# Optimization experiments

Hardware: AMD Instinct MI355X
Metric: run time of the kernel (lower is better)

## Reference

```python
import jax, jax.numpy as jnp
import numpy as np

N = 20000      # nodes (single node type)
E = 320000     # edges per relation (avg degree 16)
R = 3          # relations / edge types
L = 3          # layers
H = 4          # heads
D = 64         # dim per head (hid_size // n_heads)
IN = 256       # in_size == hid_size
OUT = 128      # out_size
NEG_SLOPE = 0.2


def setup_inputs() -> dict:
    key = jax.random.key(0)
    ks = jax.random.split(key, 8)
    x = jax.random.normal(ks[0], (N, IN), jnp.float32)
    edge_src = jax.random.randint(ks[1], (R, E), 0, N, dtype=jnp.int32)
    edge_dst = jax.random.randint(ks[2], (R, E), 0, N, dtype=jnp.int32)
    W = jax.random.normal(ks[3], (L, R, IN, H * D), jnp.float32) * (1.0 / np.sqrt(IN))
    attn_l = jax.random.normal(ks[4], (L, R, H, D), jnp.float32) * 0.1
    attn_r = jax.random.normal(ks[5], (L, R, H, D), jnp.float32) * 0.1
    bias = jnp.zeros((L, R, H * D), jnp.float32)
    fc_w = jax.random.normal(ks[6], (IN, OUT), jnp.float32) * (1.0 / np.sqrt(IN))
    fc_b = jnp.zeros((OUT,), jnp.float32)
    return dict(x=x, edge_src=edge_src, edge_dst=edge_dst, W=W,
                attn_l=attn_l, attn_r=attn_r, bias=bias, fc_w=fc_w, fc_b=fc_b)


def _gat_conv(h, src, dst, W_r, al, ar, b_r):
    # h: [N, IN] -> feat: [N, H, D]
    feat = (h @ W_r).reshape(N, H, D)
    el = jnp.sum(feat * al, axis=-1)                      # [N, H]
    er = jnp.sum(feat * ar, axis=-1)                      # [N, H]
    e = jax.nn.leaky_relu(el[src] + er[dst], NEG_SLOPE)   # [E, H]
    # segment softmax over incoming edges of each dst node, per head
    m = jax.ops.segment_max(e, dst, num_segments=N)       # [N, H]
    a = jnp.exp(e - m[dst])
    s = jax.ops.segment_sum(a, dst, num_segments=N)       # [N, H]
    alpha = a / s[dst]                                    # [E, H]
    # weighted scatter-add of source features: [N, H, D]
    out = jax.ops.segment_sum(alpha[:, :, None] * feat[src], dst, num_segments=N)
    return out + b_r.reshape(1, H, D)


def reference(x, edge_src, edge_dst, W, attn_l, attn_r, bias, fc_w, fc_b):
    h = x
    for l in range(L):
        acc = jnp.zeros((N, H, D), h.dtype)
        for r in range(R):  # sum-aggregate across relations (HeteroGraphConv aggregate='sum')
            acc = acc + _gat_conv(h, edge_src[r], edge_dst[r],
                                  W[l, r], attn_l[l, r], attn_r[l, r], bias[l, r])
        h = acc.reshape(N, H * D)
        if l != L - 1:
            h = jax.nn.relu(h)  # dropout = identity in eval
    return h @ fc_w + fc_b  # [N, OUT]
```

## Files before the change

kernel.cpp:

```cpp
#include <hip/hip_runtime.h>
#include <math.h>

#define NN 20000
#define EE 320000
#define RR 3
#define LL 3
#define HH 4
#define DD 64
#define CDIM 256
#define OUTD 128
#define NEG 0.2f

typedef float f32x4 __attribute__((ext_vector_type(4)));
typedef short sh8 __attribute__((ext_vector_type(8)));

__device__ __forceinline__ ushort f2bf(float f) {
    union { float f; uint u; } v; v.f = f;
    uint r = (v.u + 0x7FFF + ((v.u >> 16) & 1)) >> 16;
    return (ushort)r;
}
__device__ __forceinline__ float bf2f(ushort u) {
    union { uint u; float f; } v; v.u = ((uint)u) << 16;
    return v.f;
}
__device__ __forceinline__ float bflo(uint p) { return bf2f((ushort)(p & 0xffff)); }
__device__ __forceinline__ float bfhi(uint p) { return bf2f((ushort)(p >> 16)); }


__global__ void zero_ints(int* p, int n) {
    int i = blockIdx.x * blockDim.x + threadIdx.x;
    if (i < n) p[i] = 0;
}

__global__ void count_deg(const int* __restrict__ edge_dst, int* __restrict__ deg) {
    int i = blockIdx.x * blockDim.x + threadIdx.x;
    if (i >= RR * EE) return;
    int r = i / EE;
    atomicAdd(&deg[r * NN + edge_dst[i]], 1);
}

__global__ void scan_kernel(const int* __restrict__ deg, int* __restrict__ row_ptr) {
    int r = blockIdx.x;
    const int* d = deg + r * NN;
    int* rp = row_ptr + r * (NN + 1);
    __shared__ int buf[1024];
    __shared__ int carry_s;
    if (threadIdx.x == 0) { carry_s = 0; rp[0] = 0; }
    __syncthreads();
    for (int base = 0; base < NN; base += 1024) {
        int i = base + threadIdx.x;
        int v = (i < NN) ? d[i] : 0;
        buf[threadIdx.x] = v;
        __syncthreads();
        for (int off = 1; off < 1024; off <<= 1) {
            int t = (threadIdx.x >= off) ? buf[threadIdx.x - off] : 0;
            __syncthreads();
            buf[threadIdx.x] += t;
            __syncthreads();
        }
        int incl = carry_s + buf[threadIdx.x];
        if (i < NN) rp[i + 1] = incl;
        __syncthreads();
        if (threadIdx.x == 1023) carry_s = carry_s + buf[1023];
        __syncthreads();
    }
}

__global__ void fill_csr(const int* __restrict__ edge_src, const int* __restrict__ edge_dst,
                         const int* __restrict__ row_ptr, int* __restrict__ fill,
                         int* __restrict__ csr_src) {
    int i = blockIdx.x * blockDim.x + threadIdx.x;
    if (i >= RR * EE) return;
    int r = i / EE;
    int dst = edge_dst[i];
    int pos = atomicAdd(&fill[r * NN + dst], 1);
    csr_src[r * EE + row_ptr[r * (NN + 1) + dst] + pos] = edge_src[i];
}


__global__ void cvt_bf16x4(const float* __restrict__ in, ushort* __restrict__ out, int n4) {
    int i = blockIdx.x * blockDim.x + threadIdx.x;
    if (i >= n4) return;
    float4 v = *(const float4*)(in + (size_t)i * 4);
    ushort4 o;
    o.x = f2bf(v.x); o.y = f2bf(v.y); o.z = f2bf(v.z); o.w = f2bf(v.w);
    *(ushort4*)(out + (size_t)i * 4) = o;
}

__global__ void prep_Wt(const float* __restrict__ W, ushort* __restrict__ Wt, int K, int N) {
    __shared__ float tile[32][33];
    int kb = blockIdx.x * 32, nb = blockIdx.y * 32;
    size_t base = (size_t)blockIdx.z * K * N;
    for (int yy = threadIdx.y; yy < 32; yy += 8)
        tile[yy][threadIdx.x] = W[base + (size_t)(kb + yy) * N + nb + threadIdx.x];
    __syncthreads();
    for (int yy = threadIdx.y; yy < 32; yy += 8)
        Wt[base + (size_t)(nb + yy) * K + kb + threadIdx.x] = f2bf(tile[threadIdx.x][yy]);
}


#define TM 128
#define TN 128
#define TK 32
#define LP 40

__global__ __launch_bounds__(256) void gemm_bf16(
    const ushort* __restrict__ A, const ushort* __restrict__ Bt0, void* __restrict__ C0,
    int M, int K, int Ncol, long strideB, long strideC,
    const float* __restrict__ bias, int out_fp32) {
    __shared__ alignas(16) ushort As[TM * LP];
    __shared__ alignas(16) ushort Bs[TN * LP];
    const ushort* Bt = Bt0 + (size_t)blockIdx.z * strideB;
    int m0 = blockIdx.x * TM, n0 = blockIdx.y * TN;
    int t = threadIdx.x;
    int wave = t >> 6, lane = t & 63;
    int q = lane >> 4, l16 = lane & 15;
    int wrow = (wave >> 1) * 64, wcol = (wave & 1) * 64;

    f32x4 acc[4][4];
    #pragma unroll
    for (int i = 0; i < 4; i++)
        #pragma unroll
        for (int j = 0; j < 4; j++)
            #pragma unroll
            for (int k = 0; k < 4; k++) acc[i][j][k] = 0.f;

    for (int k0 = 0; k0 < K; k0 += TK) {
        #pragma unroll
        for (int s = 0; s < 2; s++) {
            int qid = t + s * 256;
            int row = qid >> 2, kq = (qid & 3) * 8;
            uint4 v = make_uint4(0, 0, 0, 0);
            int gr = m0 + row;
            if (gr < M) v = *(const uint4*)(A + (size_t)gr * K + k0 + kq);
            *(uint4*)(As + row * LP + kq) = v;
        }
        #pragma unroll
        for (int s = 0; s < 2; s++) {
            int qid = t + s * 256;
            int row = qid >> 2, kq = (qid & 3) * 8;
            uint4 v = *(const uint4*)(Bt + (size_t)(n0 + row) * K + k0 + kq);
            *(uint4*)(Bs + row * LP + kq) = v;
        }
        __syncthreads();
        sh8 af[4], bfr[4];
        #pragma unroll
        for (int i = 0; i < 4; i++)
            af[i] = *(const sh8*)(As + (wrow + i * 16 + l16) * LP + q * 8);
        #pragma unroll
        for (int j = 0; j < 4; j++)
            bfr[j] = *(const sh8*)(Bs + (wcol + j * 16 + l16) * LP + q * 8);
        #pragma unroll
        for (int i = 0; i < 4; i++)
            #pragma unroll
            for (int j = 0; j < 4; j++)
                acc[i][j] = __builtin_amdgcn_mfma_f32_16x16x32_bf16(af[i], bfr[j], acc[i][j], 0, 0, 0);
        __syncthreads();
    }

    if (out_fp32) {
        float* C = (float*)C0 + (size_t)blockIdx.z * strideC;
        #pragma unroll
        for (int i = 0; i < 4; i++) {
            #pragma unroll
            for (int reg = 0; reg < 4; reg++) {
                int row = m0 + wrow + i * 16 + q * 4 + reg;
                if (row >= M) continue;
                #pragma unroll
                for (int j = 0; j < 4; j++) {
                    int col = n0 + wcol + j * 16 + l16;
                    float v = acc[i][j][reg];
                    if (bias) v += bias[col];
                    C[(size_t)row * Ncol + col] = v;
                }
            }
        }
    } else {
        ushort* C = (ushort*)C0 + (size_t)blockIdx.z * strideC;
        #pragma unroll
        for (int i = 0; i < 4; i++) {
            #pragma unroll
            for (int reg = 0; reg < 4; reg++) {
                int row = m0 + wrow + i * 16 + q * 4 + reg;
                if (row >= M) continue;
                #pragma unroll
                for (int j = 0; j < 4; j++) {
                    int col = n0 + wcol + j * 16 + l16;
                    C[(size_t)row * Ncol + col] = f2bf(acc[i][j][reg]);
                }
            }
        }
    }
}

__global__ __launch_bounds__(256) void compute_eler(
    const ushort* __restrict__ feat16, const float* __restrict__ al,
    const float* __restrict__ ar, float* __restrict__ el, float* __restrict__ er) {
    int wave = threadIdx.x >> 6, lane = threadIdx.x & 63;
    int n = blockIdx.x * 4 + wave;
    if (n >= NN) return;
    int h = lane >> 4;
    int c = lane * 4;
    for (int r = 0; r < RR; r++) {
        const ushort* f = feat16 + ((size_t)r * NN + n) * CDIM + c;
        uint2 p = *(const uint2*)f;
        float fv[4];
        fv[0] = bflo(p.x); fv[1] = bfhi(p.x); fv[2] = bflo(p.y); fv[3] = bfhi(p.y);
        float pl = 0.f, pr = 0.f;
        #pragma unroll
        for (int i = 0; i < 4; i++) {
            pl = fmaf(fv[i], al[r * CDIM + c + i], pl);
            pr = fmaf(fv[i], ar[r * CDIM + c + i], pr);
        }
        #pragma unroll
        for (int m = 1; m < 16; m <<= 1) {
            pl += __shfl_xor(pl, m, 64);
            pr += __shfl_xor(pr, m, 64);
        }
        if ((lane & 15) == 0) {
            el[((size_t)r * NN + n) * HH + h] = pl;
            er[((size_t)r * NN + n) * HH + h] = pr;
        }
    }
}

__global__ __launch_bounds__(256) void attn_softmax(
    const float* __restrict__ el, const float* __restrict__ er,
    const int* __restrict__ row_ptr, const int* __restrict__ csr_src,
    float* __restrict__ alpha, float* __restrict__ inv_s) {
    int wv = threadIdx.x >> 6, lane = threadIdx.x & 63;
    int n = blockIdx.x * 4 + wv;
    int r = blockIdx.y;
    if (n >= NN) return;
    const int* rp = row_ptr + r * (NN + 1);
    int beg = rp[n], end = rp[n + 1];
    int h = lane & 3, eo = lane >> 2;
    float ern = er[((size_t)r * NN + n) * HH + h];
    const float* elr = el + (size_t)r * NN * HH;
    float* ar_ = alpha + (size_t)r * EE * HH;
    const int* cs = csr_src + (size_t)r * EE;
    float ssum = 0.f;
    for (int e0 = beg; e0 < end; e0 += 16) {
        int e = e0 + eo;
        float a = 0.f;
        if (e < end) {
            int s = cs[e];
            float x = elr[s * HH + h] + ern;
            x = x > 0.f ? x : NEG * x;
            a = __expf(x);
            ar_[e * HH + h] = a;
        }
        ssum += a;
    }
    ssum += __shfl_xor(ssum, 4, 64);
    ssum += __shfl_xor(ssum, 8, 64);
    ssum += __shfl_xor(ssum, 16, 64);
    ssum += __shfl_xor(ssum, 32, 64);
    if (lane < 4) inv_s[((size_t)r * NN + n) * HH + lane] = (ssum > 0.f) ? 1.f / ssum : 0.f;
}

__global__ __launch_bounds__(256) void aggregate(
    const ushort* __restrict__ feat16, const float* __restrict__ alpha,
    const float* __restrict__ inv_s, const int* __restrict__ row_ptr,
    const int* __restrict__ csr_src, const float* __restrict__ bias,
    ushort* __restrict__ hout, int relu) {
    int wv = threadIdx.x >> 6, lane = threadIdx.x & 63;
    int node = blockIdx.x * 4 + wv;
    if (node >= NN) return;
    int c0 = lane * 4;
    int h = lane >> 4;
    float t0 = 0.f, t1 = 0.f, t2 = 0.f, t3 = 0.f;
    #pragma unroll
    for (int r = 0; r < RR; r++) {
        const int* rp = row_ptr + r * (NN + 1);
        int beg = rp[node], end = rp[node + 1];
        const ushort* fr = feat16 + (size_t)r * NN * CDIM;
        const float* ar_ = alpha + (size_t)r * EE * HH;
        const int* cs = csr_src + (size_t)r * EE;
        float p0 = 0.f, p1 = 0.f, p2 = 0.f, p3 = 0.f;
        int e = beg;
        for (; e + 4 <= end; e += 4) {
            int s0 = cs[e], s1 = cs[e + 1], s2 = cs[e + 2], s3 = cs[e + 3];
            float w0 = ar_[(e + 0) * HH + h];
            float w1 = ar_[(e + 1) * HH + h];
            float w2 = ar_[(e + 2) * HH + h];
            float w3 = ar_[(e + 3) * HH + h];
            uint2 f0 = *(const uint2*)(fr + (size_t)s0 * CDIM + c0);
            uint2 f1 = *(const uint2*)(fr + (size_t)s1 * CDIM + c0);
            uint2 f2 = *(const uint2*)(fr + (size_t)s2 * CDIM + c0);
            uint2 f3 = *(const uint2*)(fr + (size_t)s3 * CDIM + c0);
            p0 = fmaf(w0, bflo(f0.x), p0); p1 = fmaf(w0, bfhi(f0.x), p1);
            p2 = fmaf(w0, bflo(f0.y), p2); p3 = fmaf(w0, bfhi(f0.y), p3);
            p0 = fmaf(w1, bflo(f1.x), p0); p1 = fmaf(w1, bfhi(f1.x), p1);
            p2 = fmaf(w1, bflo(f1.y), p2); p3 = fmaf(w1, bfhi(f1.y), p3);
            p0 = fmaf(w2, bflo(f2.x), p0); p1 = fmaf(w2, bfhi(f2.x), p1);
            p2 = fmaf(w2, bflo(f2.y), p2); p3 = fmaf(w2, bfhi(f2.y), p3);
            p0 = fmaf(w3, bflo(f3.x), p0); p1 = fmaf(w3, bfhi(f3.x), p1);
            p2 = fmaf(w3, bflo(f3.y), p2); p3 = fmaf(w3, bfhi(f3.y), p3);
        }
        for (; e < end; e++) {
            int s = cs[e];
            float w = ar_[e * HH + h];
            uint2 f = *(const uint2*)(fr + (size_t)s * CDIM + c0);
            p0 = fmaf(w, bflo(f.x), p0); p1 = fmaf(w, bfhi(f.x), p1);
            p2 = fmaf(w, bflo(f.y), p2); p3 = fmaf(w, bfhi(f.y), p3);
        }
        float is = inv_s[((size_t)r * NN + node) * HH + h];
        t0 += p0 * is + bias[r * CDIM + c0];
        t1 += p1 * is + bias[r * CDIM + c0 + 1];
        t2 += p2 * is + bias[r * CDIM + c0 + 2];
        t3 += p3 * is + bias[r * CDIM + c0 + 3];
    }
    if (relu) {
        t0 = fmaxf(t0, 0.f); t1 = fmaxf(t1, 0.f);
        t2 = fmaxf(t2, 0.f); t3 = fmaxf(t3, 0.f);
    }
    uint2 o;
    o.x = (uint)f2bf(t0) | ((uint)f2bf(t1) << 16);
    o.y = (uint)f2bf(t2) | ((uint)f2bf(t3) << 16);
    *(uint2*)(hout + (size_t)node * CDIM + c0) = o;
}


extern "C" void kernel_launch(void* const* d_in, const int* in_sizes, int n_in,
                              void* d_out, int out_size, void* d_ws, size_t ws_size,
                              hipStream_t stream) {
    const float* x        = (const float*)d_in[0];
    const int*   edge_src = (const int*)d_in[1];
    const int*   edge_dst = (const int*)d_in[2];
    const float* W        = (const float*)d_in[3];
    const float* attn_l   = (const float*)d_in[4];
    const float* attn_r   = (const float*)d_in[5];
    const float* bias     = (const float*)d_in[6];
    const float* fc_w     = (const float*)d_in[7];
    const float* fc_b     = (const float*)d_in[8];
    float* out = (float*)d_out;

    char* ws = (char*)d_ws;
    size_t off = 0;
    auto alloc = [&](size_t bytes) {
        void* p = ws + off;
        off = (off + bytes + 255) & ~(size_t)255;
        return p;
    };
    ushort* x16    = (ushort*)alloc((size_t)NN * CDIM * 2);
    ushort* h16    = (ushort*)alloc((size_t)NN * CDIM * 2);
    ushort* feat16 = (ushort*)alloc((size_t)RR * NN * CDIM * 2);
    ushort* Wt16   = (ushort*)alloc((size_t)LL * RR * CDIM * CDIM * 2);
    ushort* fct16  = (ushort*)alloc((size_t)OUTD * CDIM * 2);
    float* el      = (float*)alloc((size_t)RR * NN * HH * 4);
    float* er      = (float*)alloc((size_t)RR * NN * HH * 4);
    float* inv_s   = (float*)alloc((size_t)RR * NN * HH * 4);
    float* alpha   = (float*)alloc((size_t)RR * EE * HH * 4);
    int* row_ptr   = (int*)alloc((size_t)RR * (NN + 1) * 4);
    int* csr_src   = (int*)alloc((size_t)RR * EE * 4);
    int* deg       = (int*)alloc((size_t)2 * RR * NN * 4);
    int* fill      = deg + RR * NN;

    zero_ints<<<dim3((2 * RR * NN + 1023) / 1024), dim3(1024), 0, stream>>>(deg, 2 * RR * NN);
    count_deg<<<dim3((RR * EE + 255) / 256), dim3(256), 0, stream>>>(edge_dst, deg);
    scan_kernel<<<dim3(RR), dim3(1024), 0, stream>>>(deg, row_ptr);
    fill_csr<<<dim3((RR * EE + 255) / 256), dim3(256), 0, stream>>>(edge_src, edge_dst, row_ptr, fill, csr_src);

    cvt_bf16x4<<<dim3((NN * CDIM / 4 + 255) / 256), dim3(256), 0, stream>>>(x, x16, NN * CDIM / 4);
    prep_Wt<<<dim3(CDIM / 32, CDIM / 32, LL * RR), dim3(32, 8), 0, stream>>>(W, Wt16, CDIM, CDIM);
    prep_Wt<<<dim3(CDIM / 32, OUTD / 32, 1), dim3(32, 8), 0, stream>>>(fc_w, fct16, CDIM, OUTD);

    const ushort* hin = x16;
    for (int l = 0; l < LL; l++) {
        const ushort* Wl = Wt16 + (size_t)l * RR * CDIM * CDIM;
        dim3 g((NN + TM - 1) / TM, CDIM / TN, RR);
        gemm_bf16<<<g, dim3(256), 0, stream>>>(hin, Wl, feat16, NN, CDIM, CDIM,
                                               (long)CDIM * CDIM, (long)NN * CDIM, nullptr, 0);
        compute_eler<<<dim3(NN / 4), dim3(256), 0, stream>>>(
            feat16, attn_l + (size_t)l * RR * CDIM, attn_r + (size_t)l * RR * CDIM, el, er);
        attn_softmax<<<dim3(NN / 4, RR), dim3(256), 0, stream>>>(
            el, er, row_ptr, csr_src, alpha, inv_s);
        aggregate<<<dim3(NN / 4), dim3(256), 0, stream>>>(
            feat16, alpha, inv_s, row_ptr, csr_src, bias + (size_t)l * RR * CDIM,
            h16, (l != LL - 1) ? 1 : 0);
        hin = h16;
    }
    dim3 gf((NN + TM - 1) / TM, OUTD / TN, 1);
    gemm_bf16<<<gf, dim3(256), 0, stream>>>(h16, fct16, out, NN, CDIM, OUTD,
                                            0, 0, fc_b, 1);
}
```

Baseline: 590.5 us.

## Fuse el/er into GEMM epilogue and softmax into aggregation

The attention dot products el/er now come from the fp32 GEMM accumulators in the epilogue, using cross-lane shuffles, so the compute_eler pass that re-read feat16 is gone. The separate softmax kernel is also removed: aggregation recomputes the leaky-relu and exp per edge and divides by the running sum at the end. This drops the alpha buffer round trip (R*E*H floats written and read) and two launches per layer. The cost is extra exp work and gathers from el inside the aggregate loop, plus extra shuffles and registers in the GEMM epilogue. There is no max-subtraction, the same as the original code.

```diff
diff --git a/kernel.cpp b/kernel.cpp
--- a/kernel.cpp
+++ b/kernel.cpp
@@ -107,7 +107,9 @@
 __global__ __launch_bounds__(256) void gemm_bf16(
     const ushort* __restrict__ A, const ushort* __restrict__ Bt0, void* __restrict__ C0,
     int M, int K, int Ncol, long strideB, long strideC,
-    const float* __restrict__ bias, int out_fp32) {
+    const float* __restrict__ bias, int out_fp32,
+    const float* __restrict__ al_all, const float* __restrict__ ar_all,
+    float* __restrict__ el_all, float* __restrict__ er_all) {
     __shared__ alignas(16) ushort As[TM * LP];
     __shared__ alignas(16) ushort Bs[TN * LP];
     const ushort* Bt = Bt0 + (size_t)blockIdx.z * strideB;
@@ -191,77 +193,48 @@
             }
         }
     }
-}
-
-__global__ __launch_bounds__(256) void compute_eler(
-    const ushort* __restrict__ feat16, const float* __restrict__ al,
-    const float* __restrict__ ar, float* __restrict__ el, float* __restrict__ er) {
-    int wave = threadIdx.x >> 6, lane = threadIdx.x & 63;
-    int n = blockIdx.x * 4 + wave;
-    if (n >= NN) return;
-    int h = lane >> 4;
-    int c = lane * 4;
-    for (int r = 0; r < RR; r++) {
-        const ushort* f = feat16 + ((size_t)r * NN + n) * CDIM + c;
-        uint2 p = *(const uint2*)f;
-        float fv[4];
-        fv[0] = bflo(p.x); fv[1] = bfhi(p.x); fv[2] = bflo(p.y); fv[3] = bfhi(p.y);
-        float pl = 0.f, pr = 0.f;
+
+    if (el_all) {
+        const float* al = al_all + (size_t)blockIdx.z * CDIM;
+        const float* ar = ar_all + (size_t)blockIdx.z * CDIM;
+        float* elp = el_all + (size_t)blockIdx.z * NN * HH;
+        float* erp = er_all + (size_t)blockIdx.z * NN * HH;
+        int head = (n0 + wcol) >> 6;
+        float alj[4], arj[4];
+        #pragma unroll
+        for (int j = 0; j < 4; j++) {
+            int gcol = n0 + wcol + j * 16 + l16;
+            alj[j] = al[gcol];
+            arj[j] = ar[gcol];
+        }
         #pragma unroll
         for (int i = 0; i < 4; i++) {
-            pl = fmaf(fv[i], al[r * CDIM + c + i], pl);
-            pr = fmaf(fv[i], ar[r * CDIM + c + i], pr);
-        }
-        #pragma unroll
-        for (int m = 1; m < 16; m <<= 1) {
-            pl += __shfl_xor(pl, m, 64);
-            pr += __shfl_xor(pr, m, 64);
-        }
-        if ((lane & 15) == 0) {
-            el[((size_t)r * NN + n) * HH + h] = pl;
-            er[((size_t)r * NN + n) * HH + h] = pr;
-        }
-    }
-}
-
-__global__ __launch_bounds__(256) void attn_softmax(
-    const float* __restrict__ el, const float* __restrict__ er,
-    const int* __restrict__ row_ptr, const int* __restrict__ csr_src,
-    float* __restrict__ alpha, float* __restrict__ inv_s) {
-    int wv = threadIdx.x >> 6, lane = threadIdx.x & 63;
-    int n = blockIdx.x * 4 + wv;
-    int r = blockIdx.y;
-    if (n >= NN) return;
-    const int* rp = row_ptr + r * (NN + 1);
-    int beg = rp[n], end = rp[n + 1];
-    int h = lane & 3, eo = lane >> 2;
-    float ern = er[((size_t)r * NN + n) * HH + h];
-    const float* elr = el + (size_t)r * NN * HH;
-    float* ar_ = alpha + (size_t)r * EE * HH;
-    const int* cs = csr_src + (size_t)r * EE;
-    float ssum = 0.f;
-    for (int e0 = beg; e0 < end; e0 += 16) {
-        int e = e0 + eo;
-        float a = 0.f;
-        if (e < end) {
-            int s = cs[e];
-            float x = elr[s * HH + h] + ern;
-            x = x > 0.f ? x : NEG * x;
-            a = __expf(x);
-            ar_[e * HH + h] = a;
-        }
-        ssum += a;
-    }
-    ssum += __shfl_xor(ssum, 4, 64);
-    ssum += __shfl_xor(ssum, 8, 64);
-    ssum += __shfl_xor(ssum, 16, 64);
-    ssum += __shfl_xor(ssum, 32, 64);
-    if (lane < 4) inv_s[((size_t)r * NN + n) * HH + lane] = (ssum > 0.f) ? 1.f / ssum : 0.f;
-}
-
-__global__ __launch_bounds__(256) void aggregate(
-    const ushort* __restrict__ feat16, const float* __restrict__ alpha,
-    const float* __restrict__ inv_s, const int* __restrict__ row_ptr,
+            #pragma unroll
+            for (int reg = 0; reg < 4; reg++) {
+                int row = m0 + wrow + i * 16 + q * 4 + reg;
+                float pl = 0.f, pr = 0.f;
+                #pragma unroll
+                for (int j = 0; j < 4; j++) {
+                    pl = fmaf(acc[i][j][reg], alj[j], pl);
+                    pr = fmaf(acc[i][j][reg], arj[j], pr);
+                }
+                #pragma unroll
+                for (int m = 1; m < 16; m <<= 1) {
+                    pl += __shfl_xor(pl, m, 64);
+                    pr += __shfl_xor(pr, m, 64);
+                }
+                if (l16 == 0 && row < M) {
+                    elp[(size_t)row * HH + head] = pl;
+                    erp[(size_t)row * HH + head] = pr;
+                }
+            }
+        }
+    }
+}
+
+__global__ __launch_bounds__(256) void aggregate_fused(
+    const ushort* __restrict__ feat16, const float* __restrict__ el,
+    const float* __restrict__ er, const int* __restrict__ row_ptr,
     const int* __restrict__ csr_src, const float* __restrict__ bias,
     ushort* __restrict__ hout, int relu) {
     int wv = threadIdx.x >> 6, lane = threadIdx.x & 63;
@@ -275,37 +248,48 @@
         const int* rp = row_ptr + r * (NN + 1);
         int beg = rp[node], end = rp[node + 1];
         const ushort* fr = feat16 + (size_t)r * NN * CDIM;
-        const float* ar_ = alpha + (size_t)r * EE * HH;
+        const float* elr = el + (size_t)r * NN * HH;
+        float ern = er[((size_t)r * NN + node) * HH + h];
         const int* cs = csr_src + (size_t)r * EE;
-        float p0 = 0.f, p1 = 0.f, p2 = 0.f, p3 = 0.f;
+        float p0 = 0.f, p1 = 0.f, p2 = 0.f, p3 = 0.f, ssum = 0.f;
         int e = beg;
         for (; e + 4 <= end; e += 4) {
             int s0 = cs[e], s1 = cs[e + 1], s2 = cs[e + 2], s3 = cs[e + 3];
-            float w0 = ar_[(e + 0) * HH + h];
-            float w1 = ar_[(e + 1) * HH + h];
-            float w2 = ar_[(e + 2) * HH + h];
-            float w3 = ar_[(e + 3) * HH + h];
+            float x0 = elr[s0 * HH + h];
+            float x1 = elr[s1 * HH + h];
+            float x2 = elr[s2 * HH + h];
+            float x3 = elr[s3 * HH + h];
             uint2 f0 = *(const uint2*)(fr + (size_t)s0 * CDIM + c0);
             uint2 f1 = *(const uint2*)(fr + (size_t)s1 * CDIM + c0);
             uint2 f2 = *(const uint2*)(fr + (size_t)s2 * CDIM + c0);
             uint2 f3 = *(const uint2*)(fr + (size_t)s3 * CDIM + c0);
-            p0 = fmaf(w0, bflo(f0.x), p0); p1 = fmaf(w0, bfhi(f0.x), p1);
-            p2 = fmaf(w0, bflo(f0.y), p2); p3 = fmaf(w0, bfhi(f0.y), p3);
-            p0 = fmaf(w1, bflo(f1.x), p0); p1 = fmaf(w1, bfhi(f1.x), p1);
-            p2 = fmaf(w1, bflo(f1.y), p2); p3 = fmaf(w1, bfhi(f1.y), p3);
-            p0 = fmaf(w2, bflo(f2.x), p0); p1 = fmaf(w2, bfhi(f2.x), p1);
-            p2 = fmaf(w2, bflo(f2.y), p2); p3 = fmaf(w2, bfhi(f2.y), p3);
-            p0 = fmaf(w3, bflo(f3.x), p0); p1 = fmaf(w3, bfhi(f3.x), p1);
-            p2 = fmaf(w3, bflo(f3.y), p2); p3 = fmaf(w3, bfhi(f3.y), p3);
+            x0 += ern; x1 += ern; x2 += ern; x3 += ern;
+            x0 = x0 > 0.f ? x0 : NEG * x0;
+            x1 = x1 > 0.f ? x1 : NEG * x1;
+            x2 = x2 > 0.f ? x2 : NEG * x2;
+            x3 = x3 > 0.f ? x3 : NEG * x3;
+            float a0 = __expf(x0), a1 = __expf(x1), a2 = __expf(x2), a3 = __expf(x3);
+            ssum += a0 + a1 + a2 + a3;
+            p0 = fmaf(a0, bflo(f0.x), p0); p1 = fmaf(a0, bfhi(f0.x), p1);
+            p2 = fmaf(a0, bflo(f0.y), p2); p3 = fmaf(a0, bfhi(f0.y), p3);
+            p0 = fmaf(a1, bflo(f1.x), p0); p1 = fmaf(a1, bfhi(f1.x), p1);
+            p2 = fmaf(a1, bflo(f1.y), p2); p3 = fmaf(a1, bfhi(f1.y), p3);
+            p0 = fmaf(a2, bflo(f2.x), p0); p1 = fmaf(a2, bfhi(f2.x), p1);
+            p2 = fmaf(a2, bflo(f2.y), p2); p3 = fmaf(a2, bfhi(f2.y), p3);
+            p0 = fmaf(a3, bflo(f3.x), p0); p1 = fmaf(a3, bfhi(f3.x), p1);
+            p2 = fmaf(a3, bflo(f3.y), p2); p3 = fmaf(a3, bfhi(f3.y), p3);
         }
         for (; e < end; e++) {
             int s = cs[e];
-            float w = ar_[e * HH + h];
+            float x = elr[s * HH + h] + ern;
+            x = x > 0.f ? x : NEG * x;
+            float a = __expf(x);
             uint2 f = *(const uint2*)(fr + (size_t)s * CDIM + c0);
-            p0 = fmaf(w, bflo(f.x), p0); p1 = fmaf(w, bfhi(f.x), p1);
-            p2 = fmaf(w, bflo(f.y), p2); p3 = fmaf(w, bfhi(f.y), p3);
-        }
-        float is = inv_s[((size_t)r * NN + node) * HH + h];
+            ssum += a;
+            p0 = fmaf(a, bflo(f.x), p0); p1 = fmaf(a, bfhi(f.x), p1);
+            p2 = fmaf(a, bflo(f.y), p2); p3 = fmaf(a, bfhi(f.y), p3);
+        }
+        float is = (end > beg) ? 1.f / ssum : 0.f;
         t0 += p0 * is + bias[r * CDIM + c0];
         t1 += p1 * is + bias[r * CDIM + c0 + 1];
         t2 += p2 * is + bias[r * CDIM + c0 + 2];
@@ -350,8 +334,6 @@
     ushort* fct16  = (ushort*)alloc((size_t)OUTD * CDIM * 2);
     float* el      = (float*)alloc((size_t)RR * NN * HH * 4);
     float* er      = (float*)alloc((size_t)RR * NN * HH * 4);
-    float* inv_s   = (float*)alloc((size_t)RR * NN * HH * 4);
-    float* alpha   = (float*)alloc((size_t)RR * EE * HH * 4);
     int* row_ptr   = (int*)alloc((size_t)RR * (NN + 1) * 4);
     int* csr_src   = (int*)alloc((size_t)RR * EE * 4);
     int* deg       = (int*)alloc((size_t)2 * RR * NN * 4);
@@ -371,17 +353,15 @@
         const ushort* Wl = Wt16 + (size_t)l * RR * CDIM * CDIM;
         dim3 g((NN + TM - 1) / TM, CDIM / TN, RR);
         gemm_bf16<<<g, dim3(256), 0, stream>>>(hin, Wl, feat16, NN, CDIM, CDIM,
-                                               (long)CDIM * CDIM, (long)NN * CDIM, nullptr, 0);
-        compute_eler<<<dim3(NN / 4), dim3(256), 0, stream>>>(
-            feat16, attn_l + (size_t)l * RR * CDIM, attn_r + (size_t)l * RR * CDIM, el, er);
-        attn_softmax<<<dim3(NN / 4, RR), dim3(256), 0, stream>>>(
-            el, er, row_ptr, csr_src, alpha, inv_s);
-        aggregate<<<dim3(NN / 4), dim3(256), 0, stream>>>(
-            feat16, alpha, inv_s, row_ptr, csr_src, bias + (size_t)l * RR * CDIM,
+                                               (long)CDIM * CDIM, (long)NN * CDIM, nullptr, 0,
+                                               attn_l + (size_t)l * RR * CDIM,
+                                               attn_r + (size_t)l * RR * CDIM, el, er);
+        aggregate_fused<<<dim3(NN / 4), dim3(256), 0, stream>>>(
+            feat16, el, er, row_ptr, csr_src, bias + (size_t)l * RR * CDIM,
             h16, (l != LL - 1) ? 1 : 0);
         hin = h16;
     }
     dim3 gf((NN + TM - 1) / TM, OUTD / TN, 1);
     gemm_bf16<<<gf, dim3(256), 0, stream>>>(h16, fct16, out, NN, CDIM, OUTD,
-                                            0, 0, fc_b, 1);
-}
+                                            0, 0, fc_b, 1, nullptr, nullptr, nullptr, nullptr);
+}
```

Result: faster. 537.6 us (-9.0%).
